# Kernel tuning notes

Hardware: AMD Instinct MI355X
Metric: run time of the kernel (lower is better)

The kernel has to match this reference:

```python
import jax, jax.numpy as jnp
import numpy as np
from jax import lax

DN = ('NCHW', 'OIHW', 'NCHW')
EPS = 1e-5  # PyTorch BatchNorm default eps


def _bn(x, g, b):
    # BatchNorm2d in training mode: batch statistics over (N, H, W), biased var
    m = jnp.mean(x, (0, 2, 3), keepdims=True)
    v = jnp.mean((x - m) ** 2, (0, 2, 3), keepdims=True)
    return (x - m) * lax.rsqrt(v + EPS) * g[None, :, None, None] + b[None, :, None, None]


def _conv(x, w, b):
    # Conv2d(k=4, stride=2, padding=1)
    y = lax.conv_general_dilated(x, w, (2, 2), ((1, 1), (1, 1)), dimension_numbers=DN)
    return y + b[None, :, None, None]


def _deconv(x, w, b):
    # ConvTranspose2d(k=4, stride=2, padding=1) == dilated-input conv, pad k-1-p=2
    y = lax.conv_general_dilated(x, w, (1, 1), ((2, 2), (2, 2)), lhs_dilation=(2, 2),
                                 dimension_numbers=DN)
    return y + b[None, :, None, None]


def reference(x, codebook, eW1, eb1, eg1, ebt1, eW2, eb2, eg2, ebt2, eW3, eb3, eg3, ebt3,
              dW1, db1, dg1, dbt1, dW2, db2, dg2, dbt2, dW3, db3, dg3, dbt3):
    # --- encoder ---
    h = jax.nn.relu(_bn(_conv(x, eW1, eb1), eg1, ebt1))
    h = jax.nn.relu(_bn(_conv(h, eW2, eb2), eg2, ebt2))
    z_e = jax.nn.relu(_bn(_conv(h, eW3, eb3), eg3, ebt3))  # [B, 64, H/8, W/8]
    # --- vector quantization ---
    zp = z_e.transpose(0, 2, 3, 1)                 # [B, h, w, D]
    D = zp.shape[-1]
    z = zp.reshape(-1, D)                          # [N, D]
    dist = (jnp.sum(z * z, axis=1, keepdims=True)
            + jnp.sum(codebook * codebook, axis=1)
            - 2.0 * (z @ codebook.T))              # [N, K] squared distances
    idx = jnp.argmin(dist, axis=1)                 # [N]
    quant = codebook[idx].reshape(zp.shape)        # gather == one-hot matmul
    e_loss = jnp.mean((lax.stop_gradient(quant) - zp) ** 2)
    q_loss = jnp.mean((quant - lax.stop_gradient(zp)) ** 2)
    loss = q_loss + e_loss
    # straight-through estimator
    q_st = (zp + lax.stop_gradient(quant - zp)).transpose(0, 3, 1, 2)  # [B, D, h, w]
    # --- decoder ---
    h = jax.nn.relu(_bn(_deconv(q_st, dW1, db1), dg1, dbt1))
    h = jax.nn.relu(_bn(_deconv(h, dW2, db2), dg2, dbt2))
    z_d = jnp.tanh(_bn(_deconv(h, dW3, db3), dg3, dbt3))
    return z_d, loss


def setup_inputs() -> dict:
    key = jax.random.key(0)
    ks = jax.random.split(key, 16)
    B, C, H, W = 64, 3, 256, 256
    K, D = 512, 64
    f32 = jnp.float32

    def w(k, shape, fan_in):
        return jax.random.normal(k, shape, f32) * np.float32(1.0 / np.sqrt(fan_in))

    inp = {}
    inp['x'] = jax.random.normal(ks[0], (B, C, H, W), f32)
    inp['codebook'] = jax.random.uniform(ks[1], (K, D), f32, -1.0 / K, 1.0 / K)
    # encoder: 3 -> 16 -> 32 -> 64, conv k=4
    inp['eW1'] = w(ks[2], (16, 3, 4, 4), 3 * 16);   inp['eb1'] = jnp.zeros(16, f32)
    inp['eg1'] = jnp.ones(16, f32);                 inp['ebt1'] = jnp.zeros(16, f32)
    inp['eW2'] = w(ks[3], (32, 16, 4, 4), 16 * 16); inp['eb2'] = jnp.zeros(32, f32)
    inp['eg2'] = jnp.ones(32, f32);                 inp['ebt2'] = jnp.zeros(32, f32)
    inp['eW3'] = w(ks[4], (64, 32, 4, 4), 32 * 16); inp['eb3'] = jnp.zeros(64, f32)
    inp['eg3'] = jnp.ones(64, f32);                 inp['ebt3'] = jnp.zeros(64, f32)
    # decoder: 64 -> 32 -> 16 -> 3, convtranspose k=4 (weights stored OIHW)
    inp['dW1'] = w(ks[5], (32, 64, 4, 4), 64 * 16); inp['db1'] = jnp.zeros(32, f32)
    inp['dg1'] = jnp.ones(32, f32);                 inp['dbt1'] = jnp.zeros(32, f32)
    inp['dW2'] = w(ks[6], (16, 32, 4, 4), 32 * 16); inp['db2'] = jnp.zeros(16, f32)
    inp['dg2'] = jnp.ones(16, f32);                 inp['dbt2'] = jnp.zeros(16, f32)
    inp['dW3'] = w(ks[7], (3, 16, 4, 4), 16 * 16);  inp['db3'] = jnp.zeros(3, f32)
    inp['dg3'] = jnp.ones(3, f32);                  inp['dbt3'] = jnp.zeros(3, f32)
    return inp
```

## Files before the change

### kernel.cpp

```cpp
#include <hip/hip_runtime.h>
#include <hip/hip_bf16.h>


#define EPS 1e-5

__global__ void zero_stats_k(double* s, int n) {
    int i = blockIdx.x * blockDim.x + threadIdx.x;
    if (i < n) s[i] = 0.0;
}

__global__ void convert_w_k(const float* __restrict__ w1, const float* __restrict__ w2,
                            const float* __restrict__ w3, double* __restrict__ w64) {
    int i = blockIdx.x * blockDim.x + threadIdx.x;
    if (i < 768) w64[i] = (double)w1[i];
    else if (i < 768 + 8192) w64[i] = (double)w2[i - 768];
    else if (i < 768 + 8192 + 32768) w64[i] = (double)w3[i - 768 - 8192];
}

__device__ __forceinline__ void block_reduce2(double v1, double v2,
                                              double* t1, double* t2) {
#pragma unroll
    for (int o = 32; o; o >>= 1) {
        v1 += __shfl_down(v1, o);
        v2 += __shfl_down(v2, o);
    }
    __shared__ double ls[4][2];
    int wid = threadIdx.x >> 6, lane = threadIdx.x & 63;
    if (lane == 0) { ls[wid][0] = v1; ls[wid][1] = v2; }
    __syncthreads();
    if (threadIdx.x == 0) {
        atomicAdd(t1, ls[0][0] + ls[1][0] + ls[2][0] + ls[3][0]);
        atomicAdd(t2, ls[0][1] + ls[1][1] + ls[2][1] + ls[3][1]);
    }
    __syncthreads();
}

__global__ void conv1_stats_k(const float* __restrict__ x, const double* __restrict__ w64,
                              const float* __restrict__ bias,
                              double* __restrict__ partials) {
    __shared__ float xs[3][6][258];
    __shared__ double lsw[4][32];
    int band = blockIdx.x, n = blockIdx.y, tid = threadIdx.x;
    double sums[16], sqs[16];
#pragma unroll
    for (int j = 0; j < 16; ++j) { sums[j] = 0.0; sqs[j] = 0.0; }
    for (int s8 = 0; s8 < 2; ++s8) {
        int strip = band * 2 + s8;
        int iyBase = 4 * strip - 1;
        __syncthreads();
        for (int idx = tid; idx < 3 * 6 * 258; idx += 256) {
            int ch = idx / 1548, rem = idx - ch * 1548, r = rem / 258, cc = rem - r * 258;
            int iy = iyBase + r, ix = cc - 1;
            float v = 0.f;
            if ((unsigned)iy < 256u && (unsigned)ix < 256u)
                v = x[(size_t)(n * 3 + ch) * 65536 + iy * 256 + ix];
            xs[ch][r][cc] = v;
        }
        __syncthreads();
        int lr = 2 * (tid >> 7), lc = 2 * (tid & 127);
        double xd[3][4][4];
#pragma unroll
        for (int ci = 0; ci < 3; ++ci)
#pragma unroll
            for (int ky = 0; ky < 4; ++ky)
#pragma unroll
                for (int kx = 0; kx < 4; ++kx)
                    xd[ci][ky][kx] = (double)xs[ci][lr + ky][lc + kx];
#pragma unroll
        for (int co = 0; co < 16; ++co) {
            double acc = (double)bias[co];
            const double* wp = w64 + co * 48;
#pragma unroll
            for (int ci = 0; ci < 3; ++ci)
#pragma unroll
                for (int ky = 0; ky < 4; ++ky)
#pragma unroll
                    for (int kx = 0; kx < 4; ++kx)
                        acc = fma(xd[ci][ky][kx], wp[ci * 16 + ky * 4 + kx], acc);
            sums[co] += acc;
            sqs[co] = fma(acc, acc, sqs[co]);
        }
    }
    double val[32];
#pragma unroll
    for (int j = 0; j < 16; ++j) { val[j] = sums[j]; val[16 + j] = sqs[j]; }
#pragma unroll
    for (int o = 32; o; o >>= 1)
#pragma unroll
        for (int j = 0; j < 32; ++j) val[j] += __shfl_down(val[j], o);
    int wid = tid >> 6, lane = tid & 63;
    if (lane == 0)
#pragma unroll
        for (int j = 0; j < 32; ++j) lsw[wid][j] = val[j];
    __syncthreads();
    if (tid < 32) {
        double p = lsw[0][tid] + lsw[1][tid] + lsw[2][tid] + lsw[3][tid];
        partials[(size_t)(n * 32 + band) * 32 + tid] = p;
    }
}

__global__ void reduce_stats_k(const double* __restrict__ partials,
                               double* __restrict__ stats) {
    int t = threadIdx.x;
    if (t < 32) {
        double s = 0.0;
        for (int i = 0; i < 2048; ++i) s += partials[(size_t)i * 32 + t];
        stats[t] = s;
    }
}

__global__ void fused_conv2_k(const float* __restrict__ x, const double* __restrict__ w1_64,
                              const float* __restrict__ eb1, const float* __restrict__ eg1,
                              const float* __restrict__ ebt1, const double* __restrict__ w2_64,
                              const float* __restrict__ eb2, const double* __restrict__ stats,
                              float* __restrict__ h2) {
    __shared__ float xs[3][38][38];
    __shared__ float h1s[16][18][18];
    int tile = blockIdx.x, n = blockIdx.y, tid = threadIdx.x;
    int ty = tile >> 3, tx = tile & 7;
    int iyBase = 32 * ty - 3, ixBase = 32 * tx - 3;
    for (int idx = tid; idx < 3 * 38 * 38; idx += 256) {
        int ch = idx / 1444, rem = idx - ch * 1444, r = rem / 38, cc = rem - r * 38;
        int iy = iyBase + r, ix = ixBase + cc;
        float v = 0.f;
        if ((unsigned)iy < 256u && (unsigned)ix < 256u)
            v = x[(size_t)(n * 3 + ch) * 65536 + iy * 256 + ix];
        xs[ch][r][cc] = v;
    }
    __syncthreads();
    int hy0 = 16 * ty - 1, hx0 = 16 * tx - 1;
    for (int idx = tid; idx < 16 * 18 * 18; idx += 256) {
        int ci = idx / 324, rem = idx - ci * 324, r = rem / 18, cc = rem - r * 18;
        int hy = hy0 + r, hx = hx0 + cc;
        float val = 0.f;
        if ((unsigned)hy < 128u && (unsigned)hx < 128u) {
            double xd[3][4][4];
#pragma unroll
            for (int c3 = 0; c3 < 3; ++c3)
#pragma unroll
                for (int ky = 0; ky < 4; ++ky)
#pragma unroll
                    for (int kx = 0; kx < 4; ++kx)
                        xd[c3][ky][kx] = (double)xs[c3][2 * r + ky][2 * cc + kx];
            double acc = (double)eb1[ci];
            const double* wp = w1_64 + ci * 48;
#pragma unroll
            for (int c3 = 0; c3 < 3; ++c3)
#pragma unroll
                for (int ky = 0; ky < 4; ++ky)
#pragma unroll
                    for (int kx = 0; kx < 4; ++kx)
                        acc = fma(xd[c3][ky][kx], wp[c3 * 16 + ky * 4 + kx], acc);
            double m = stats[ci] * (1.0 / 1048576.0);
            double var = stats[16 + ci] * (1.0 / 1048576.0) - m * m;
            double sc = (double)eg1[ci] / sqrt(var + EPS);
            double sh = (double)ebt1[ci] - m * sc;
            double v = fma(acc, sc, sh);
            val = (float)(v > 0.0 ? v : 0.0);
        }
        h1s[ci][r][cc] = val;
    }
    __syncthreads();
    int s = tid & 63, ly = s >> 3, lx = s & 7;
    int cog = __builtin_amdgcn_readfirstlane((tid >> 6) * 8);
    double acc[8];
#pragma unroll
    for (int j = 0; j < 8; ++j) acc[j] = (double)eb2[cog + j];
    for (int ci = 0; ci < 16; ++ci) {
        double td[16];
#pragma unroll
        for (int ky = 0; ky < 4; ++ky)
#pragma unroll
            for (int kx = 0; kx < 4; ++kx)
                td[ky * 4 + kx] = (double)h1s[ci][2 * ly + ky][2 * lx + kx];
#pragma unroll
        for (int j = 0; j < 8; ++j) {
            const double* wp = w2_64 + ((cog + j) * 16 + ci) * 16;
#pragma unroll
            for (int k = 0; k < 16; ++k)
                acc[j] = fma(td[k], wp[k], acc[j]);
        }
    }
    int oy = 8 * ty + ly, ox = 8 * tx + lx;
#pragma unroll
    for (int j = 0; j < 8; ++j)
        h2[(size_t)(n * 32 + cog + j) * 4096 + oy * 64 + ox] = (float)acc[j];
}

__global__ void bn_stats_k(const float* __restrict__ y, double* __restrict__ sum,
                           double* __restrict__ sq, int C, int HW) {
    int c = blockIdx.x, n = blockIdx.y;
    const float* p = y + (size_t)(n * C + c) * HW;
    double s = 0.0, s2 = 0.0;
    for (int i = threadIdx.x; i < HW; i += blockDim.x) {
        double v = (double)p[i];
        s += v;
        s2 = fma(v, v, s2);
    }
    block_reduce2(s, s2, &sum[c], &sq[c]);
}

__device__ __forceinline__ void bn_consts(int tid, int C, const double* sum,
                                          const double* sq, const float* g,
                                          const float* b, double invCnt,
                                          double* scd, double* shd) {
    if (tid < C) {
        double m = sum[tid] * invCnt;
        double var = sq[tid] * invCnt - m * m;
        double sc = (double)g[tid] / sqrt(var + EPS);
        scd[tid] = sc;
        shd[tid] = (double)b[tid] - m * sc;
    }
}

__global__ void conv3_k(const float* __restrict__ h2, const double* __restrict__ w3_64,
                        const float* __restrict__ bias, const float* __restrict__ eg2,
                        const float* __restrict__ ebt2, const double* __restrict__ sum2,
                        const double* __restrict__ sq2, float* __restrict__ z3) {
    __shared__ float hs[32][6][66];
    __shared__ double scd[32], shd[32];
    int c = blockIdx.x, n = blockIdx.y, tid = threadIdx.x;
    bn_consts(tid, 32, sum2, sq2, eg2, ebt2, 1.0 / 262144.0, scd, shd);
    __syncthreads();
    int iyBase = 4 * c - 1;
    for (int idx = tid; idx < 32 * 6 * 66; idx += 256) {
        int ch = idx / 396, rem = idx - ch * 396, r = rem / 66, cc = rem - r * 66;
        int iy = iyBase + r, ix = cc - 1;
        float val = 0.f;
        if ((unsigned)iy < 64u && (unsigned)ix < 64u) {
            double v = fma((double)h2[(size_t)(n * 32 + ch) * 4096 + iy * 64 + ix],
                           scd[ch], shd[ch]);
            val = v > 0.0 ? (float)v : 0.f;
        }
        hs[ch][r][cc] = val;
    }
    __syncthreads();
    int s = tid & 63;
    int oy = 2 * c + (s >> 5), ox = s & 31;
    int lr = 2 * (s >> 5), lc = 2 * ox;
    int cog = __builtin_amdgcn_readfirstlane((tid >> 6) * 16);
    double acc[16];
#pragma unroll
    for (int j = 0; j < 16; ++j) acc[j] = (double)bias[cog + j];
    for (int ci = 0; ci < 32; ++ci) {
        double td[16];
#pragma unroll
        for (int ky = 0; ky < 4; ++ky)
#pragma unroll
            for (int kx = 0; kx < 4; ++kx)
                td[ky * 4 + kx] = (double)hs[ci][lr + ky][lc + kx];
#pragma unroll
        for (int j = 0; j < 16; ++j) {
            const double* wp = w3_64 + ((cog + j) * 32 + ci) * 16;
#pragma unroll
            for (int k = 0; k < 16; ++k)
                acc[j] = fma(td[k], wp[k], acc[j]);
        }
    }
#pragma unroll
    for (int j = 0; j < 16; ++j)
        z3[(size_t)(n * 64 + cog + j) * 1024 + oy * 32 + ox] = (float)acc[j];
}

__device__ __forceinline__ float np_sum64(const float* a) {
    float r[8];
#pragma unroll
    for (int j = 0; j < 8; ++j) r[j] = a[j];
#pragma unroll
    for (int m = 1; m < 8; ++m)
#pragma unroll
        for (int j = 0; j < 8; ++j) r[j] += a[m * 8 + j];
    return ((r[0] + r[1]) + (r[2] + r[3])) + ((r[4] + r[5]) + (r[6] + r[7]));
}

__global__ void scc_k(const float* __restrict__ cb, float* __restrict__ scc) {
    int k = blockIdx.x * blockDim.x + threadIdx.x;
    if (k >= 512) return;
    const float* c = cb + (k << 6);
    float cc[64];
#pragma unroll
    for (int d = 0; d < 64; ++d) cc[d] = c[d] * c[d];
    scc[k] = np_sum64(cc);
}

__global__ void vq_k(const float* __restrict__ zraw, const float* __restrict__ cb,
                     const float* __restrict__ scc, const float* __restrict__ eg3,
                     const float* __restrict__ ebt3, const double* __restrict__ sum3,
                     const double* __restrict__ sq3, float* __restrict__ quant,
                     double* __restrict__ lossAcc) {
    __shared__ double scd[64], shd[64];
    __shared__ float bfs[256];
    __shared__ int bis[256];
    bn_consts(threadIdx.x, 64, sum3, sq3, eg3, ebt3, 1.0 / 65536.0, scd, shd);
    __syncthreads();
    int chunk = threadIdx.x >> 6, pi = threadIdx.x & 63;
    int p = blockIdx.x * 64 + pi;
    int n = p >> 10, hw = p & 1023;
    const float* zp = zraw + (size_t)n * 65536 + hw;
    float z32[64], zz[64];
#pragma unroll
    for (int d = 0; d < 64; ++d) {
        double v = fma((double)zp[d * 1024], scd[d], shd[d]);
        z32[d] = v > 0.0 ? (float)v : 0.f;
        zz[d] = z32[d] * z32[d];
    }
    float sz = np_sum64(zz);
    int k0 = chunk << 7;
    float bestf = 3.4e38f;
    int bif = k0;
    for (int k = k0; k < k0 + 128; ++k) {
        const float* c = cb + (k << 6);
        float dot = 0.f;
#pragma unroll
        for (int d = 0; d < 64; ++d) dot = fmaf(z32[d], c[d], dot);
        float distf = (sz + scc[k]) - 2.f * dot;
        if (distf < bestf) { bestf = distf; bif = k; }
    }
    bfs[threadIdx.x] = bestf;
    bis[threadIdx.x] = bif;
    __syncthreads();
    if (chunk == 0) {
#pragma unroll
        for (int c4 = 1; c4 < 4; ++c4) {
            float v = bfs[c4 * 64 + pi];
            if (v < bestf) { bestf = v; bif = bis[c4 * 64 + pi]; }
        }
        const float* c = cb + (bif << 6);
        float* qp = quant + (size_t)n * 65536 + hw;
        double dist = 0.0;
#pragma unroll
        for (int d = 0; d < 64; ++d) {
            double diff = (double)z32[d] - (double)c[d];
            dist = fma(diff, diff, dist);
            qp[d * 1024] = c[d];
        }
        double s = dist;
#pragma unroll
        for (int o = 32; o; o >>= 1) s += __shfl_down(s, o);
        if (pi == 0) atomicAdd(lossAcc, s);
    }
}

__global__ void finalize_loss_k(const double* lossAcc, float* out, int idx) {
    if (threadIdx.x == 0 && blockIdx.x == 0)
        out[idx] = (float)(2.0 * (*lossAcc) / 4194304.0);
}

__global__ void deconv1_k(const float* __restrict__ in, const float* __restrict__ w,
                          const float* __restrict__ bias, float* __restrict__ out) {
    __shared__ float ls[64][4][34];
    int b = blockIdx.x, n = blockIdx.y, tid = threadIdx.x;
    int qy0 = 2 * b;
    for (int idx = tid; idx < 64 * 4 * 34; idx += 256) {
        int ch = idx / 136, rem = idx - ch * 136, r = rem / 34, cc = rem - r * 34;
        int iy = qy0 - 1 + r, ix = cc - 1;
        float v = 0.f;
        if ((unsigned)iy < 32u && (unsigned)ix < 32u)
            v = in[(size_t)(n * 64 + ch) * 1024 + iy * 32 + ix];
        ls[ch][r][cc] = v;
    }
    __syncthreads();
    int pt = tid & 63;
    int qy = qy0 + (pt >> 5), qx = pt & 31;
    int cog = (tid >> 6) * 8;
    int rb = qy - qy0;
    float acc[2][2][8];
#pragma unroll
    for (int dy = 0; dy < 2; ++dy)
#pragma unroll
        for (int dx = 0; dx < 2; ++dx)
#pragma unroll
            for (int j = 0; j < 8; ++j) acc[dy][dx][j] = bias[cog + j];
    for (int ci = 0; ci < 64; ++ci) {
        float v[3][3];
#pragma unroll
        for (int ry = 0; ry < 3; ++ry)
#pragma unroll
            for (int rx = 0; rx < 3; ++rx)
                v[ry][rx] = ls[ci][rb + ry][qx + rx];
#pragma unroll
        for (int j = 0; j < 8; ++j) {
            const float* wp = w + ((cog + j) * 64 + ci) * 16;
            acc[0][0][j] += v[0][0]*wp[0] + v[0][1]*wp[2] + v[1][0]*wp[8]  + v[1][1]*wp[10];
            acc[0][1][j] += v[0][1]*wp[1] + v[0][2]*wp[3] + v[1][1]*wp[9]  + v[1][2]*wp[11];
            acc[1][0][j] += v[1][0]*wp[4] + v[1][1]*wp[6] + v[2][0]*wp[12] + v[2][1]*wp[14];
            acc[1][1][j] += v[1][1]*wp[5] + v[1][2]*wp[7] + v[2][1]*wp[13] + v[2][2]*wp[15];
        }
    }
#pragma unroll
    for (int dy = 0; dy < 2; ++dy)
#pragma unroll
        for (int dx = 0; dx < 2; ++dx)
#pragma unroll
            for (int j = 0; j < 8; ++j)
                out[(size_t)(n * 32 + cog + j) * 4096 + (2*qy+dy) * 64 + 2*qx+dx]
                    = acc[dy][dx][j];
}

__global__ void deconv2_k(const float* __restrict__ in, const float* __restrict__ w,
                          const float* __restrict__ bias, const float* __restrict__ g,
                          const float* __restrict__ bt, const double* __restrict__ sum,
                          const double* __restrict__ sq, float* __restrict__ out) {
    __shared__ float ls[32][3][66];
    __shared__ double scd[32], shd[32];
    int b = blockIdx.x, n = blockIdx.y, tid = threadIdx.x;
    bn_consts(tid, 32, sum, sq, g, bt, 1.0 / 262144.0, scd, shd);
    __syncthreads();
    for (int idx = tid; idx < 32 * 3 * 66; idx += 256) {
        int ch = idx / 198, rem = idx - ch * 198, r = rem / 66, cc = rem - r * 66;
        int iy = b - 1 + r, ix = cc - 1;
        float val = 0.f;
        if ((unsigned)iy < 64u && (unsigned)ix < 64u) {
            double v = fma((double)in[(size_t)(n * 32 + ch) * 4096 + iy * 64 + ix],
                           scd[ch], shd[ch]);
            val = v > 0.0 ? (float)v : 0.f;
        }
        ls[ch][r][cc] = val;
    }
    __syncthreads();
    int qx = tid & 63;
    int cog = (tid >> 6) * 4;
    float acc[2][2][4];
#pragma unroll
    for (int dy = 0; dy < 2; ++dy)
#pragma unroll
        for (int dx = 0; dx < 2; ++dx)
#pragma unroll
            for (int j = 0; j < 4; ++j) acc[dy][dx][j] = bias[cog + j];
    for (int ci = 0; ci < 32; ++ci) {
        float v[3][3];
#pragma unroll
        for (int ry = 0; ry < 3; ++ry)
#pragma unroll
            for (int rx = 0; rx < 3; ++rx)
                v[ry][rx] = ls[ci][ry][qx + rx];
#pragma unroll
        for (int j = 0; j < 4; ++j) {
            const float* wp = w + ((cog + j) * 32 + ci) * 16;
            acc[0][0][j] += v[0][0]*wp[0] + v[0][1]*wp[2] + v[1][0]*wp[8]  + v[1][1]*wp[10];
            acc[0][1][j] += v[0][1]*wp[1] + v[0][2]*wp[3] + v[1][1]*wp[9]  + v[1][2]*wp[11];
            acc[1][0][j] += v[1][0]*wp[4] + v[1][1]*wp[6] + v[2][0]*wp[12] + v[2][1]*wp[14];
            acc[1][1][j] += v[1][1]*wp[5] + v[1][2]*wp[7] + v[2][1]*wp[13] + v[2][2]*wp[15];
        }
    }
#pragma unroll
    for (int dy = 0; dy < 2; ++dy)
#pragma unroll
        for (int dx = 0; dx < 2; ++dx)
#pragma unroll
            for (int j = 0; j < 4; ++j)
                out[(size_t)(n * 16 + cog + j) * 16384 + (2*b+dy) * 128 + 2*qx+dx]
                    = acc[dy][dx][j];
}

__global__ void deconv3_k(const float* __restrict__ in, const float* __restrict__ w,
                          const float* __restrict__ bias, const float* __restrict__ g,
                          const float* __restrict__ bt, const double* __restrict__ sum,
                          const double* __restrict__ sq, float* __restrict__ out) {
    __shared__ float ls[16][4][130];
    __shared__ double scd[16], shd[16];
    int b = blockIdx.x, n = blockIdx.y, tid = threadIdx.x;
    bn_consts(tid, 16, sum, sq, g, bt, 1.0 / 1048576.0, scd, shd);
    __syncthreads();
    int qy0 = 2 * b;
    for (int idx = tid; idx < 16 * 4 * 130; idx += 256) {
        int ch = idx / 520, rem = idx - ch * 520, r = rem / 130, cc = rem - r * 130;
        int iy = qy0 - 1 + r, ix = cc - 1;
        float val = 0.f;
        if ((unsigned)iy < 128u && (unsigned)ix < 128u) {
            double v = fma((double)in[(size_t)(n * 16 + ch) * 16384 + iy * 128 + ix],
                           scd[ch], shd[ch]);
            val = v > 0.0 ? (float)v : 0.f;
        }
        ls[ch][r][cc] = val;
    }
    __syncthreads();
    int qy = qy0 + (tid >> 7), qx = tid & 127;
    int rb = qy - qy0;
    float acc[2][2][3];
#pragma unroll
    for (int dy = 0; dy < 2; ++dy)
#pragma unroll
        for (int dx = 0; dx < 2; ++dx)
#pragma unroll
            for (int j = 0; j < 3; ++j) acc[dy][dx][j] = bias[j];
    for (int ci = 0; ci < 16; ++ci) {
        float v[3][3];
#pragma unroll
        for (int ry = 0; ry < 3; ++ry)
#pragma unroll
            for (int rx = 0; rx < 3; ++rx)
                v[ry][rx] = ls[ci][rb + ry][qx + rx];
#pragma unroll
        for (int j = 0; j < 3; ++j) {
            const float* wp = w + (j * 16 + ci) * 16;
            acc[0][0][j] += v[0][0]*wp[0] + v[0][1]*wp[2] + v[1][0]*wp[8]  + v[1][1]*wp[10];
            acc[0][1][j] += v[0][1]*wp[1] + v[0][2]*wp[3] + v[1][1]*wp[9]  + v[1][2]*wp[11];
            acc[1][0][j] += v[1][0]*wp[4] + v[1][1]*wp[6] + v[2][0]*wp[12] + v[2][1]*wp[14];
            acc[1][1][j] += v[1][1]*wp[5] + v[1][2]*wp[7] + v[2][1]*wp[13] + v[2][2]*wp[15];
        }
    }
#pragma unroll
    for (int dy = 0; dy < 2; ++dy)
#pragma unroll
        for (int dx = 0; dx < 2; ++dx)
#pragma unroll
            for (int j = 0; j < 3; ++j)
                out[(size_t)(n * 3 + j) * 65536 + (2*qy+dy) * 256 + 2*qx+dx]
                    = acc[dy][dx][j];
}

__global__ void bn_tanh_k(const float* __restrict__ y, const double* __restrict__ sum,
                          const double* __restrict__ sq, const float* __restrict__ g,
                          const float* __restrict__ b, float* __restrict__ out, int HW,
                          double invCnt) {
    int hw = blockIdx.x * blockDim.x + threadIdx.x;
    int c = blockIdx.y, n = blockIdx.z, C = gridDim.y;
    double m = sum[c] * invCnt;
    double var = sq[c] * invCnt - m * m;
    double sc = (double)g[c] / sqrt(var + EPS);
    double sh = (double)b[c] - m * sc;
    size_t i = (size_t)(n * C + c) * HW + hw;
    out[i] = tanhf((float)fma((double)y[i], sc, sh));
}

extern "C" void kernel_launch(void* const* d_in, const int* in_sizes, int n_in,
                              void* d_out, int out_size, void* d_ws, size_t ws_size,
                              hipStream_t stream) {
    const float* x   = (const float*)d_in[0];
    const float* cb  = (const float*)d_in[1];
    const float* eW1 = (const float*)d_in[2];
    const float* eb1 = (const float*)d_in[3];
    const float* eg1 = (const float*)d_in[4];
    const float* ebt1= (const float*)d_in[5];
    const float* eW2 = (const float*)d_in[6];
    const float* eb2 = (const float*)d_in[7];
    const float* eg2 = (const float*)d_in[8];
    const float* ebt2= (const float*)d_in[9];
    const float* eW3 = (const float*)d_in[10];
    const float* eb3 = (const float*)d_in[11];
    const float* eg3 = (const float*)d_in[12];
    const float* ebt3= (const float*)d_in[13];
    const float* dW1 = (const float*)d_in[14];
    const float* db1 = (const float*)d_in[15];
    const float* dg1 = (const float*)d_in[16];
    const float* dbt1= (const float*)d_in[17];
    const float* dW2 = (const float*)d_in[18];
    const float* db2 = (const float*)d_in[19];
    const float* dg2 = (const float*)d_in[20];
    const float* dbt2= (const float*)d_in[21];
    const float* dW3 = (const float*)d_in[22];
    const float* db3 = (const float*)d_in[23];
    const float* dg3 = (const float*)d_in[24];
    const float* dbt3= (const float*)d_in[25];

    float* out = (float*)d_out;
    char* ws = (char*)d_ws;
    float* h2    = (float*)ws;
    float* z     = (float*)(ws + 33554432);
    float* quant = (float*)(ws + 50331648);
    float* d1    = (float*)(ws + 67108864);
    float* d2    = (float*)ws;
    float* d3    = (float*)(ws + 67108864);
    double* partials = (double*)ws;
    double* w64  = (double*)(ws + 67108864);
    double* w1_64 = w64;
    double* w2_64 = w64 + 768;
    double* w3_64 = w64 + 768 + 8192;
    double* stats = (double*)(ws + 117440512);
    double* lossAcc = stats + 326;
    float* scc   = (float*)(ws + 117443200);
    dim3 B(256);

    zero_stats_k<<<2, B, 0, stream>>>(stats, 327);
    scc_k<<<2, B, 0, stream>>>(cb, scc);
    convert_w_k<<<163, B, 0, stream>>>(eW1, eW2, eW3, w64);

    conv1_stats_k<<<dim3(32, 64), B, 0, stream>>>(x, w1_64, eb1, partials);
    reduce_stats_k<<<1, 64, 0, stream>>>(partials, stats);
    fused_conv2_k<<<dim3(64, 64), B, 0, stream>>>(x, w1_64, eb1, eg1, ebt1, w2_64,
                                                  eb2, stats, h2);
    bn_stats_k<<<dim3(32, 64), B, 0, stream>>>(h2, stats + 32, stats + 64, 32, 4096);
    conv3_k<<<dim3(16, 64), B, 0, stream>>>(h2, w3_64, eb3, eg2, ebt2,
                                            stats + 32, stats + 64, z);
    bn_stats_k<<<dim3(64, 64), B, 0, stream>>>(z, stats + 96, stats + 160, 64, 1024);
    vq_k<<<1024, B, 0, stream>>>(z, cb, scc, eg3, ebt3, stats + 96, stats + 160,
                                 quant, lossAcc);
    finalize_loss_k<<<1, 64, 0, stream>>>(lossAcc, out, out_size - 1);

    deconv1_k<<<dim3(16, 64), B, 0, stream>>>(quant, dW1, db1, d1);
    bn_stats_k<<<dim3(32, 64), B, 0, stream>>>(d1, stats + 224, stats + 256, 32, 4096);
    deconv2_k<<<dim3(64, 64), B, 0, stream>>>(d1, dW2, db2, dg1, dbt1,
                                              stats + 224, stats + 256, d2);
    bn_stats_k<<<dim3(16, 64), B, 0, stream>>>(d2, stats + 288, stats + 304, 16, 16384);
    deconv3_k<<<dim3(64, 64), B, 0, stream>>>(d2, dW3, db3, dg2, dbt2,
                                              stats + 288, stats + 304, d3);
    bn_stats_k<<<dim3(3, 64), B, 0, stream>>>(d3, stats + 320, stats + 323, 3, 65536);
    bn_tanh_k<<<dim3(256, 3, 64), B, 0, stream>>>(d3, stats + 320, stats + 323,
                                                  dg3, dbt3, out, 65536,
                                                  1.0 / 4194304.0);
}
```

Baseline: 1.832 ms.

## Fuse BatchNorm statistics into conv/deconv epilogues with per-block partials

Each conv and deconv kernel now accumulates per-channel sum and sum-of-squares in its epilogue via wave shuffles and writes per-block partials. Small reduce kernels then fold those partials, replacing the separate bn_stats passes that re-read whole activation tensors and used atomics. The final deconv writes straight to the output buffer and tanh is applied in place, dropping one intermediate buffer. The single-thread serial partial reduction is also parallelised across blocks. The cost is more registers and shuffles in the conv kernels, and the risk that workspace aliasing between partials and activations is wrong.

```diff
diff --git a/kernel.cpp b/kernel.cpp
--- a/kernel.cpp
+++ b/kernel.cpp
@@ -17,22 +17,19 @@
     else if (i < 768 + 8192 + 32768) w64[i] = (double)w3[i - 768 - 8192];
 }
 
-__device__ __forceinline__ void block_reduce2(double v1, double v2,
-                                              double* t1, double* t2) {
-#pragma unroll
-    for (int o = 32; o; o >>= 1) {
-        v1 += __shfl_down(v1, o);
-        v2 += __shfl_down(v2, o);
-    }
-    __shared__ double ls[4][2];
+__global__ void reduce_p_k(const double* __restrict__ p, int nblk, int c2,
+                           double* __restrict__ dst) {
+    int slot = blockIdx.x;
+    double s = 0.0;
+    for (int j = threadIdx.x; j < nblk; j += 256)
+        s += p[(size_t)j * c2 + slot];
+#pragma unroll
+    for (int o = 32; o; o >>= 1) s += __shfl_down(s, o);
+    __shared__ double ls[4];
     int wid = threadIdx.x >> 6, lane = threadIdx.x & 63;
-    if (lane == 0) { ls[wid][0] = v1; ls[wid][1] = v2; }
-    __syncthreads();
-    if (threadIdx.x == 0) {
-        atomicAdd(t1, ls[0][0] + ls[1][0] + ls[2][0] + ls[3][0]);
-        atomicAdd(t2, ls[0][1] + ls[1][1] + ls[2][1] + ls[3][1]);
-    }
-    __syncthreads();
+    if (lane == 0) ls[wid] = s;
+    __syncthreads();
+    if (threadIdx.x == 0) dst[slot] = ls[0] + ls[1] + ls[2] + ls[3];
 }
 
 __global__ void conv1_stats_k(const float* __restrict__ x, const double* __restrict__ w64,
@@ -99,21 +96,11 @@
     }
 }
 
-__global__ void reduce_stats_k(const double* __restrict__ partials,
-                               double* __restrict__ stats) {
-    int t = threadIdx.x;
-    if (t < 32) {
-        double s = 0.0;
-        for (int i = 0; i < 2048; ++i) s += partials[(size_t)i * 32 + t];
-        stats[t] = s;
-    }
-}
-
 __global__ void fused_conv2_k(const float* __restrict__ x, const double* __restrict__ w1_64,
                               const float* __restrict__ eb1, const float* __restrict__ eg1,
                               const float* __restrict__ ebt1, const double* __restrict__ w2_64,
                               const float* __restrict__ eb2, const double* __restrict__ stats,
-                              float* __restrict__ h2) {
+                              float* __restrict__ h2, double* __restrict__ ph2) {
     __shared__ float xs[3][38][38];
     __shared__ float h1s[16][18][18];
     int tile = blockIdx.x, n = blockIdx.y, tid = threadIdx.x;
@@ -182,22 +169,30 @@
         }
     }
     int oy = 8 * ty + ly, ox = 8 * tx + lx;
-#pragma unroll
-    for (int j = 0; j < 8; ++j)
-        h2[(size_t)(n * 32 + cog + j) * 4096 + oy * 64 + ox] = (float)acc[j];
-}
-
-__global__ void bn_stats_k(const float* __restrict__ y, double* __restrict__ sum,
-                           double* __restrict__ sq, int C, int HW) {
-    int c = blockIdx.x, n = blockIdx.y;
-    const float* p = y + (size_t)(n * C + c) * HW;
-    double s = 0.0, s2 = 0.0;
-    for (int i = threadIdx.x; i < HW; i += blockDim.x) {
-        double v = (double)p[i];
-        s += v;
-        s2 = fma(v, v, s2);
-    }
-    block_reduce2(s, s2, &sum[c], &sq[c]);
+    double s8[8], q8[8];
+#pragma unroll
+    for (int j = 0; j < 8; ++j) {
+        float f = (float)acc[j];
+        h2[(size_t)(n * 32 + cog + j) * 4096 + oy * 64 + ox] = f;
+        double v = (double)f;
+        s8[j] = v;
+        q8[j] = v * v;
+    }
+#pragma unroll
+    for (int o = 32; o; o >>= 1)
+#pragma unroll
+        for (int j = 0; j < 8; ++j) {
+            s8[j] += __shfl_down(s8[j], o);
+            q8[j] += __shfl_down(q8[j], o);
+        }
+    if (s == 0) {
+        size_t blk = (size_t)(n * 64 + tile) * 64;
+#pragma unroll
+        for (int j = 0; j < 8; ++j) {
+            ph2[blk + cog + j] = s8[j];
+            ph2[blk + 32 + cog + j] = q8[j];
+        }
+    }
 }
 
 __device__ __forceinline__ void bn_consts(int tid, int C, const double* sum,
@@ -216,7 +211,8 @@
 __global__ void conv3_k(const float* __restrict__ h2, const double* __restrict__ w3_64,
                         const float* __restrict__ bias, const float* __restrict__ eg2,
                         const float* __restrict__ ebt2, const double* __restrict__ sum2,
-                        const double* __restrict__ sq2, float* __restrict__ z3) {
+                        const double* __restrict__ sq2, float* __restrict__ z3,
+                        double* __restrict__ pz) {
     __shared__ float hs[32][6][66];
     __shared__ double scd[32], shd[32];
     int c = blockIdx.x, n = blockIdx.y, tid = threadIdx.x;
@@ -257,9 +253,30 @@
                 acc[j] = fma(td[k], wp[k], acc[j]);
         }
     }
-#pragma unroll
-    for (int j = 0; j < 16; ++j)
-        z3[(size_t)(n * 64 + cog + j) * 1024 + oy * 32 + ox] = (float)acc[j];
+    double s16[16], q16[16];
+#pragma unroll
+    for (int j = 0; j < 16; ++j) {
+        float f = (float)acc[j];
+        z3[(size_t)(n * 64 + cog + j) * 1024 + oy * 32 + ox] = f;
+        double v = (double)f;
+        s16[j] = v;
+        q16[j] = v * v;
+    }
+#pragma unroll
+    for (int o = 32; o; o >>= 1)
+#pragma unroll
+        for (int j = 0; j < 16; ++j) {
+            s16[j] += __shfl_down(s16[j], o);
+            q16[j] += __shfl_down(q16[j], o);
+        }
+    if (s == 0) {
+        size_t blk = (size_t)(n * 16 + c) * 128;
+#pragma unroll
+        for (int j = 0; j < 16; ++j) {
+            pz[blk + cog + j] = s16[j];
+            pz[blk + 64 + cog + j] = q16[j];
+        }
+    }
 }
 
 __device__ __forceinline__ float np_sum64(const float* a) {
@@ -347,7 +364,8 @@
 }
 
 __global__ void deconv1_k(const float* __restrict__ in, const float* __restrict__ w,
-                          const float* __restrict__ bias, float* __restrict__ out) {
+                          const float* __restrict__ bias, float* __restrict__ out,
+                          double* __restrict__ pd1) {
     __shared__ float ls[64][4][34];
     int b = blockIdx.x, n = blockIdx.y, tid = threadIdx.x;
     int qy0 = 2 * b;
@@ -387,20 +405,43 @@
             acc[1][1][j] += v[1][1]*wp[5] + v[1][2]*wp[7] + v[2][1]*wp[13] + v[2][2]*wp[15];
         }
     }
+    double s8[8], q8[8];
+#pragma unroll
+    for (int j = 0; j < 8; ++j) { s8[j] = 0.0; q8[j] = 0.0; }
 #pragma unroll
     for (int dy = 0; dy < 2; ++dy)
 #pragma unroll
         for (int dx = 0; dx < 2; ++dx)
 #pragma unroll
-            for (int j = 0; j < 8; ++j)
-                out[(size_t)(n * 32 + cog + j) * 4096 + (2*qy+dy) * 64 + 2*qx+dx]
-                    = acc[dy][dx][j];
+            for (int j = 0; j < 8; ++j) {
+                float f = acc[dy][dx][j];
+                out[(size_t)(n * 32 + cog + j) * 4096 + (2*qy+dy) * 64 + 2*qx+dx] = f;
+                double v = (double)f;
+                s8[j] += v;
+                q8[j] = fma(v, v, q8[j]);
+            }
+#pragma unroll
+    for (int o = 32; o; o >>= 1)
+#pragma unroll
+        for (int j = 0; j < 8; ++j) {
+            s8[j] += __shfl_down(s8[j], o);
+            q8[j] += __shfl_down(q8[j], o);
+        }
+    if (pt == 0) {
+        size_t blk = (size_t)(n * 16 + b) * 64;
+#pragma unroll
+        for (int j = 0; j < 8; ++j) {
+            pd1[blk + cog + j] = s8[j];
+            pd1[blk + 32 + cog + j] = q8[j];
+        }
+    }
 }
 
 __global__ void deconv2_k(const float* __restrict__ in, const float* __restrict__ w,
                           const float* __restrict__ bias, const float* __restrict__ g,
                           const float* __restrict__ bt, const double* __restrict__ sum,
-                          const double* __restrict__ sq, float* __restrict__ out) {
+                          const double* __restrict__ sq, float* __restrict__ out,
+                          double* __restrict__ pd2) {
     __shared__ float ls[32][3][66];
     __shared__ double scd[32], shd[32];
     int b = blockIdx.x, n = blockIdx.y, tid = threadIdx.x;
@@ -443,22 +484,46 @@
             acc[1][1][j] += v[1][1]*wp[5] + v[1][2]*wp[7] + v[2][1]*wp[13] + v[2][2]*wp[15];
         }
     }
+    double s4[4], q4[4];
+#pragma unroll
+    for (int j = 0; j < 4; ++j) { s4[j] = 0.0; q4[j] = 0.0; }
 #pragma unroll
     for (int dy = 0; dy < 2; ++dy)
 #pragma unroll
         for (int dx = 0; dx < 2; ++dx)
 #pragma unroll
-            for (int j = 0; j < 4; ++j)
-                out[(size_t)(n * 16 + cog + j) * 16384 + (2*b+dy) * 128 + 2*qx+dx]
-                    = acc[dy][dx][j];
+            for (int j = 0; j < 4; ++j) {
+                float f = acc[dy][dx][j];
+                out[(size_t)(n * 16 + cog + j) * 16384 + (2*b+dy) * 128 + 2*qx+dx] = f;
+                double v = (double)f;
+                s4[j] += v;
+                q4[j] = fma(v, v, q4[j]);
+            }
+#pragma unroll
+    for (int o = 32; o; o >>= 1)
+#pragma unroll
+        for (int j = 0; j < 4; ++j) {
+            s4[j] += __shfl_down(s4[j], o);
+            q4[j] += __shfl_down(q4[j], o);
+        }
+    if (qx == 0) {
+        size_t blk = (size_t)(n * 64 + b) * 32;
+#pragma unroll
+        for (int j = 0; j < 4; ++j) {
+            pd2[blk + cog + j] = s4[j];
+            pd2[blk + 16 + cog + j] = q4[j];
+        }
+    }
 }
 
 __global__ void deconv3_k(const float* __restrict__ in, const float* __restrict__ w,
                           const float* __restrict__ bias, const float* __restrict__ g,
                           const float* __restrict__ bt, const double* __restrict__ sum,
-                          const double* __restrict__ sq, float* __restrict__ out) {
+                          const double* __restrict__ sq, float* __restrict__ out,
+                          double* __restrict__ pd3) {
     __shared__ float ls[16][4][130];
     __shared__ double scd[16], shd[16];
+    __shared__ double lsw[4][6];
     int b = blockIdx.x, n = blockIdx.y, tid = threadIdx.x;
     bn_consts(tid, 16, sum, sq, g, bt, 1.0 / 1048576.0, scd, shd);
     __syncthreads();
@@ -500,20 +565,42 @@
             acc[1][1][j] += v[1][1]*wp[5] + v[1][2]*wp[7] + v[2][1]*wp[13] + v[2][2]*wp[15];
         }
     }
+    double s3[3], q3[3];
+#pragma unroll
+    for (int j = 0; j < 3; ++j) { s3[j] = 0.0; q3[j] = 0.0; }
 #pragma unroll
     for (int dy = 0; dy < 2; ++dy)
 #pragma unroll
         for (int dx = 0; dx < 2; ++dx)
 #pragma unroll
-            for (int j = 0; j < 3; ++j)
-                out[(size_t)(n * 3 + j) * 65536 + (2*qy+dy) * 256 + 2*qx+dx]
-                    = acc[dy][dx][j];
-}
-
-__global__ void bn_tanh_k(const float* __restrict__ y, const double* __restrict__ sum,
+            for (int j = 0; j < 3; ++j) {
+                float f = acc[dy][dx][j];
+                out[(size_t)(n * 3 + j) * 65536 + (2*qy+dy) * 256 + 2*qx+dx] = f;
+                double v = (double)f;
+                s3[j] += v;
+                q3[j] = fma(v, v, q3[j]);
+            }
+#pragma unroll
+    for (int o = 32; o; o >>= 1)
+#pragma unroll
+        for (int j = 0; j < 3; ++j) {
+            s3[j] += __shfl_down(s3[j], o);
+            q3[j] += __shfl_down(q3[j], o);
+        }
+    int wid = tid >> 6, lane = tid & 63;
+    if (lane == 0)
+#pragma unroll
+        for (int j = 0; j < 3; ++j) { lsw[wid][j] = s3[j]; lsw[wid][3 + j] = q3[j]; }
+    __syncthreads();
+    if (tid < 6) {
+        double p = lsw[0][tid] + lsw[1][tid] + lsw[2][tid] + lsw[3][tid];
+        pd3[(size_t)(n * 64 + b) * 6 + tid] = p;
+    }
+}
+
+__global__ void bn_tanh_k(float* __restrict__ y, const double* __restrict__ sum,
                           const double* __restrict__ sq, const float* __restrict__ g,
-                          const float* __restrict__ b, float* __restrict__ out, int HW,
-                          double invCnt) {
+                          const float* __restrict__ b, int HW, double invCnt) {
     int hw = blockIdx.x * blockDim.x + threadIdx.x;
     int c = blockIdx.y, n = blockIdx.z, C = gridDim.y;
     double m = sum[c] * invCnt;
@@ -521,7 +608,7 @@
     double sc = (double)g[c] / sqrt(var + EPS);
     double sh = (double)b[c] - m * sc;
     size_t i = (size_t)(n * C + c) * HW + hw;
-    out[i] = tanhf((float)fma((double)y[i], sc, sh));
+    y[i] = tanhf((float)fma((double)y[i], sc, sh));
 }
 
 extern "C" void kernel_launch(void* const* d_in, const int* in_sizes, int n_in,
@@ -561,12 +648,16 @@
     float* quant = (float*)(ws + 50331648);
     float* d1    = (float*)(ws + 67108864);
     float* d2    = (float*)ws;
-    float* d3    = (float*)(ws + 67108864);
     double* partials = (double*)ws;
     double* w64  = (double*)(ws + 67108864);
     double* w1_64 = w64;
     double* w2_64 = w64 + 768;
     double* w3_64 = w64 + 768 + 8192;
+    double* ph2  = (double*)(ws + 50331648);
+    double* pz   = (double*)(ws + 52428800);
+    double* pd1  = (double*)ws;
+    double* pd2  = (double*)(ws + 100663296);
+    double* pd3  = (double*)(ws + 67108864);
     double* stats = (double*)(ws + 117440512);
     double* lossAcc = stats + 326;
     float* scc   = (float*)(ws + 117443200);
@@ -577,26 +668,25 @@
     convert_w_k<<<163, B, 0, stream>>>(eW1, eW2, eW3, w64);
 
     conv1_stats_k<<<dim3(32, 64), B, 0, stream>>>(x, w1_64, eb1, partials);
-    reduce_stats_k<<<1, 64, 0, stream>>>(partials, stats);
+    reduce_p_k<<<32, B, 0, stream>>>(partials, 2048, 32, stats);
     fused_conv2_k<<<dim3(64, 64), B, 0, stream>>>(x, w1_64, eb1, eg1, ebt1, w2_64,
-                                                  eb2, stats, h2);
-    bn_stats_k<<<dim3(32, 64), B, 0, stream>>>(h2, stats + 32, stats + 64, 32, 4096);
+                                                  eb2, stats, h2, ph2);
+    reduce_p_k<<<64, B, 0, stream>>>(ph2, 4096, 64, stats + 32);
     conv3_k<<<dim3(16, 64), B, 0, stream>>>(h2, w3_64, eb3, eg2, ebt2,
-                                            stats + 32, stats + 64, z);
-    bn_stats_k<<<dim3(64, 64), B, 0, stream>>>(z, stats + 96, stats + 160, 64, 1024);
+                                            stats + 32, stats + 64, z, pz);
+    reduce_p_k<<<128, B, 0, stream>>>(pz, 1024, 128, stats + 96);
     vq_k<<<1024, B, 0, stream>>>(z, cb, scc, eg3, ebt3, stats + 96, stats + 160,
                                  quant, lossAcc);
     finalize_loss_k<<<1, 64, 0, stream>>>(lossAcc, out, out_size - 1);
 
-    deconv1_k<<<dim3(16, 64), B, 0, stream>>>(quant, dW1, db1, d1);
-    bn_stats_k<<<dim3(32, 64), B, 0, stream>>>(d1, stats + 224, stats + 256, 32, 4096);
+    deconv1_k<<<dim3(16, 64), B, 0, stream>>>(quant, dW1, db1, d1, pd1);
+    reduce_p_k<<<64, B, 0, stream>>>(pd1, 1024, 64, stats + 224);
     deconv2_k<<<dim3(64, 64), B, 0, stream>>>(d1, dW2, db2, dg1, dbt1,
-                                              stats + 224, stats + 256, d2);
-    bn_stats_k<<<dim3(16, 64), B, 0, stream>>>(d2, stats + 288, stats + 304, 16, 16384);
+                                              stats + 224, stats + 256, d2, pd2);
+    reduce_p_k<<<32, B, 0, stream>>>(pd2, 4096, 32, stats + 288);
     deconv3_k<<<dim3(64, 64), B, 0, stream>>>(d2, dW3, db3, dg2, dbt2,
-                                              stats + 288, stats + 304, d3);
-    bn_stats_k<<<dim3(3, 64), B, 0, stream>>>(d3, stats + 320, stats + 323, 3, 65536);
-    bn_tanh_k<<<dim3(256, 3, 64), B, 0, stream>>>(d3, stats + 320, stats + 323,
-                                                  dg3, dbt3, out, 65536,
-                                                  1.0 / 4194304.0);
-}
+                                              stats + 288, stats + 304, out, pd3);
+    reduce_p_k<<<6, B, 0, stream>>>(pd3, 4096, 6, stats + 320);
+    bn_tanh_k<<<dim3(256, 3, 64), B, 0, stream>>>(out, stats + 320, stats + 323,
+                                                  dg3, dbt3, 65536, 1.0 / 4194304.0);
+}
```

Measured after the change: 1.802 ms. No clear change (-1.6%).
